# Optimization experiments

Hardware: AMD Instinct MI355X
Metric: run time of the kernel (lower is better)

The kernel has to match this reference:

```python
import jax, jax.numpy as jnp
import numpy as np

EMBED = 2048
HEADS = 16
GROUPS = 4
HEAD_DIM = EMBED // HEADS  # 128
REPEATS = HEADS // GROUPS  # 4


def setup_inputs() -> dict:
    key = jax.random.key(0)
    ks = jax.random.split(key, 9)
    s = 1.0 / np.sqrt(EMBED)
    kv_dim = GROUPS * HEAD_DIM
    return {
        "x": jax.random.normal(ks[0], (2, 2048, EMBED), dtype=jnp.float32),
        "Wq": jax.random.normal(ks[1], (EMBED, EMBED), dtype=jnp.float32) * s,
        "bq": jnp.zeros((EMBED,), dtype=jnp.float32),
        "Wk": jax.random.normal(ks[2], (EMBED, kv_dim), dtype=jnp.float32) * s,
        "bk": jnp.zeros((kv_dim,), dtype=jnp.float32),
        "Wv": jax.random.normal(ks[3], (EMBED, kv_dim), dtype=jnp.float32) * s,
        "bv": jnp.zeros((kv_dim,), dtype=jnp.float32),
        "Wo": jax.random.normal(ks[4], (EMBED, EMBED), dtype=jnp.float32) * s,
        "bo": jnp.zeros((EMBED,), dtype=jnp.float32),
    }


def reference(x, Wq, bq, Wk, bk, Wv, bv, Wo, bo):
    b, t, e = x.shape
    q = x @ Wq + bq                                   # [b,t,e]
    k = x @ Wk + bk                                   # [b,t,g*d]
    v = x @ Wv + bv
    # [b, g, r, t, d] for q; [b, g, t, d] for k,v (repeat_interleave == group-major)
    q = q.reshape(b, t, GROUPS, REPEATS, HEAD_DIM).transpose(0, 2, 3, 1, 4)
    k = k.reshape(b, t, GROUPS, HEAD_DIM).transpose(0, 2, 1, 3)
    v = v.reshape(b, t, GROUPS, HEAD_DIM).transpose(0, 2, 1, 3)
    scale = 1.0 / np.sqrt(HEAD_DIM)
    scores = jnp.einsum('bgrqd,bgkd->bgrqk', q, k) * scale
    causal = jnp.tril(jnp.ones((t, t), dtype=bool))
    scores = jnp.where(causal, scores, -jnp.inf)
    w = jax.nn.softmax(scores, axis=-1)
    out = jnp.einsum('bgrqk,bgkd->bgrqd', w, v)       # [b,g,r,t,d]
    out = out.transpose(0, 3, 1, 2, 4).reshape(b, t, e)
    return out @ Wo + bo
```

## Files before the change

kernel.cpp:

```cpp
#include <hip/hip_runtime.h>
#include <cstdint>

typedef __bf16 bf16;
typedef __attribute__((ext_vector_type(8))) __bf16 bf16x8;
typedef __attribute__((ext_vector_type(4))) __bf16 bf16x4;
typedef __attribute__((ext_vector_type(4))) float f32x4;
typedef __attribute__((ext_vector_type(4))) short short4_t;

__device__ __forceinline__ void load_lds16(const void* g, void* l) {
  __builtin_amdgcn_global_load_lds(
      (const __attribute__((address_space(1))) unsigned int*)g,
      (__attribute__((address_space(3))) unsigned int*)l, 16, 0, 0);
}

__device__ __forceinline__ float fast_exp2(float x) {
  float r;
  asm volatile("v_exp_f32 %0, %1" : "=v"(r) : "v"(x));
  return r;
}

template <bool OUT_F32>
__global__ __launch_bounds__(256) void gemm_bt(
    const bf16* __restrict__ A, const bf16* __restrict__ Bt,
    const float* __restrict__ bias, void* __restrict__ Cv,
    int M, int N, int K) {
  __shared__ __align__(16) bf16 sA[128 * 64];
  __shared__ __align__(16) bf16 sB[128 * 64];
  const int t = threadIdx.x;
  const int w = t >> 6, lane = t & 63;
  const int quad = lane >> 4, l16 = lane & 15;
  const int wm = (w >> 1) * 64, wn = (w & 1) * 64;
  const int nbx = gridDim.x;
  const int nwg = nbx * gridDim.y;
  const int orig = blockIdx.y * nbx + blockIdx.x;
  const int id = (orig & 7) * (nwg >> 3) + (orig >> 3);
  const int bm = (id / nbx) * 128, bn = (id % nbx) * 128;

  f32x4 acc[4][4] = {};
  const int srow = lane >> 3;
  const int sg = lane & 7;

  for (int kt = 0; kt < (K >> 6); ++kt) {
    const int k0 = kt << 6;
#pragma unroll
    for (int c2 = 0; c2 < 4; ++c2) {
      int c = c2 * 4 + w;
      int row = c * 8 + srow;
      int gg = sg ^ (row & 7);
      load_lds16(A + (int64_t)(bm + row) * K + k0 + gg * 8, sA + c * 512);
      load_lds16(Bt + (int64_t)(bn + row) * K + k0 + gg * 8, sB + c * 512);
    }
    asm volatile("s_waitcnt vmcnt(0)" ::: "memory");
    __syncthreads();
#pragma unroll
    for (int ks = 0; ks < 2; ++ks) {
      bf16x8 af[4], bfr[4];
#pragma unroll
      for (int i = 0; i < 4; ++i) {
        int m = wm + i * 16 + l16;
        af[i] = *(const bf16x8*)(sA + m * 64 + (((ks * 4 + quad) ^ (l16 & 7)) * 8));
        int n = wn + i * 16 + l16;
        bfr[i] = *(const bf16x8*)(sB + n * 64 + (((ks * 4 + quad) ^ (l16 & 7)) * 8));
      }
#pragma unroll
      for (int i = 0; i < 4; ++i)
#pragma unroll
        for (int j = 0; j < 4; ++j)
          acc[i][j] = __builtin_amdgcn_mfma_f32_16x16x32_bf16(af[i], bfr[j],
                                                              acc[i][j], 0, 0, 0);
    }
    __syncthreads();
  }
#pragma unroll
  for (int i = 0; i < 4; ++i) {
    int gm = bm + wm + i * 16 + quad * 4;
#pragma unroll
    for (int j = 0; j < 4; ++j) {
      int gn = bn + wn + j * 16 + l16;
      float bvv = bias ? bias[gn] : 0.0f;
#pragma unroll
      for (int r = 0; r < 4; ++r) {
        float v = acc[i][j][r] + bvv;
        if (OUT_F32)
          ((float*)Cv)[(int64_t)(gm + r) * N + gn] = v;
        else
          ((bf16*)Cv)[(int64_t)(gm + r) * N + gn] = (bf16)v;
      }
    }
  }
}

__global__ __launch_bounds__(256, 2) void attn(
    const bf16* __restrict__ QKV, const bf16* __restrict__ Vt,
    bf16* __restrict__ Out) {
  constexpr float CC = 0.08838834764831845f * 1.44269504088896f;
  __shared__ __align__(16) bf16 sK[2][64 * 128];
  __shared__ __align__(16) bf16 sV[2][128 * 64];

  const int t = threadIdx.x;
  const int w = t >> 6, lane = t & 63;
  const int quad = lane >> 4, l16 = lane & 15;
  const int h = blockIdx.y, b = blockIdx.z;
  const int p = (b == 0) ? (int)blockIdx.x : 15 - (int)blockIdx.x;
  const int g = h >> 2;
  const int wr0 = w * 16;
  const int kbase = 2048 + g * 128;
  const bf16* vtb = Vt + (int64_t)((b * 4 + g) * 128) * 2048;
  const int rk = lane >> 4, rv = lane >> 3, sgv = lane & 7;
  const int qrow0A = p * 64, qrow0B = (31 - p) * 64;
  const int niters = 32 - p;

  auto stage = [&](int n0, bf16* sKb, bf16* sVb) {
#pragma unroll
    for (int c2 = 0; c2 < 4; ++c2) {
      int c = c2 * 4 + w;
      int rowk = c * 4 + rk;
      int ggk = (l16 & 8) | ((l16 ^ rowk) & 7);
      load_lds16(QKV + (int64_t)(b * 2048 + n0 + rowk) * 3072 + kbase + ggk * 8,
                 sKb + c * 512);
      int rowv = c * 8 + rv;
      int ggv = sgv ^ (rowv & 7);
      load_lds16(vtb + (int64_t)rowv * 2048 + n0 + ggv * 8, sVb + c * 512);
    }
  };

  stage(0, sK[0], sV[0]);

  bf16x8 qreg[2][4];
#pragma unroll
  for (int u = 0; u < 2; ++u) {
    int qr = (u == 0 ? qrow0A : qrow0B);
#pragma unroll
    for (int ks = 0; ks < 4; ++ks) {
      bf16x8 v = *(const bf16x8*)(QKV +
          (int64_t)(b * 2048 + qr + wr0 + l16) * 3072 + h * 128 + ks * 32 +
          quad * 8);
#pragma unroll
      for (int e = 0; e < 8; ++e) v[e] = (bf16)((float)v[e] * CC);
      qreg[u][ks] = v;
    }
  }

  f32x4 oacc[2][8] = {};
  float mrow[2] = {-3.0e38f, -3.0e38f};
  float lrow[2] = {0.f, 0.f};

  for (int it = 0; it < niters; ++it) {
    const int cur = it & 1;
    const int n0 = it * 64;
    bf16* sKc = sK[cur];
    bf16* sVc = sV[cur];
    const bool actA = (it <= p);

    asm volatile("s_waitcnt vmcnt(0)\n\ts_barrier" ::: "memory");
    if (it + 1 < niters) stage(n0 + 64, sK[cur ^ 1], sV[cur ^ 1]);

    f32x4 sacc[2][4] = {};
    if (actA) {
#pragma unroll
      for (int ks = 0; ks < 4; ++ks) {
        bf16x8 ak[4];
#pragma unroll
        for (int mj = 0; mj < 4; ++mj) {
          int kvr = mj * 16 + l16;
          int G = ks * 4 + quad;
          int slot = (G & 8) | ((G ^ kvr) & 7);
          ak[mj] = *(const bf16x8*)(sKc + kvr * 128 + slot * 8);
        }
        __builtin_amdgcn_s_setprio(1);
#pragma unroll
        for (int mj = 0; mj < 4; ++mj) {
          sacc[0][mj] = __builtin_amdgcn_mfma_f32_16x16x32_bf16(
              ak[mj], qreg[0][ks], sacc[0][mj], 0, 0, 0);
          sacc[1][mj] = __builtin_amdgcn_mfma_f32_16x16x32_bf16(
              ak[mj], qreg[1][ks], sacc[1][mj], 0, 0, 0);
        }
        __builtin_amdgcn_s_setprio(0);
      }
    } else {
#pragma unroll
      for (int ks = 0; ks < 4; ++ks) {
        bf16x8 ak[4];
#pragma unroll
        for (int mj = 0; mj < 4; ++mj) {
          int kvr = mj * 16 + l16;
          int G = ks * 4 + quad;
          int slot = (G & 8) | ((G ^ kvr) & 7);
          ak[mj] = *(const bf16x8*)(sKc + kvr * 128 + slot * 8);
        }
        __builtin_amdgcn_s_setprio(1);
#pragma unroll
        for (int mj = 0; mj < 4; ++mj)
          sacc[1][mj] = __builtin_amdgcn_mfma_f32_16x16x32_bf16(
              ak[mj], qreg[1][ks], sacc[1][mj], 0, 0, 0);
        __builtin_amdgcn_s_setprio(0);
      }
    }

    short4_t pb[2][4];
    auto softmax_u = [&](int u, bool last, int qrow0u) {
      if (last) {
        int qg = qrow0u + wr0 + l16;
#pragma unroll
        for (int mj = 0; mj < 4; ++mj)
#pragma unroll
          for (int r = 0; r < 4; ++r) {
            int kv = n0 + mj * 16 + quad * 4 + r;
            if (kv > qg) sacc[u][mj][r] = -3.0e38f;
          }
      }
      f32x4 m01, m23;
#pragma unroll
      for (int r = 0; r < 4; ++r) {
        m01[r] = fmaxf(sacc[u][0][r], sacc[u][1][r]);
        m23[r] = fmaxf(sacc[u][2][r], sacc[u][3][r]);
      }
      float mx = fmaxf(fmaxf(fmaxf(m01[0], m01[1]), fmaxf(m01[2], m01[3])),
                       fmaxf(fmaxf(m23[0], m23[1]), fmaxf(m23[2], m23[3])));
      mx = fmaxf(mx, __shfl_xor(mx, 16));
      mx = fmaxf(mx, __shfl_xor(mx, 32));
      if (!__all(mx <= mrow[u] + 11.0f)) {
        float mnew = fmaxf(mrow[u], mx);
        float alpha = fast_exp2(mrow[u] - mnew);
        lrow[u] *= alpha;
#pragma unroll
        for (int dj = 0; dj < 8; ++dj)
#pragma unroll
          for (int r = 0; r < 4; ++r) oacc[u][dj][r] *= alpha;
        mrow[u] = mnew;
      }
      float rs = 0.f;
#pragma unroll
      for (int mj = 0; mj < 4; ++mj) {
        bf16x4 p4;
#pragma unroll
        for (int r = 0; r < 4; ++r) {
          float pv = fast_exp2(sacc[u][mj][r] - mrow[u]);
          rs += pv;
          p4[r] = (bf16)pv;
        }
        pb[u][mj] = __builtin_bit_cast(short4_t, p4);
      }
      rs += __shfl_xor(rs, 16);
      rs += __shfl_xor(rs, 32);
      lrow[u] += rs;
    };
    if (actA) softmax_u(0, it == p, qrow0A);
    softmax_u(1, it == niters - 1, qrow0B);

#pragma unroll
    for (int mj = 0; mj < 4; ++mj) {
      const int sbase = mj * 2 + (quad >> 1);
      const int soff = (quad & 1) * 4;
      short4_t av[8];
#pragma unroll
      for (int dj = 0; dj < 8; ++dj) {
        int d = dj * 16 + l16;
        av[dj] = *(const short4_t*)(sVc + d * 64 + ((sbase ^ (d & 7)) * 8) + soff);
      }
      __builtin_amdgcn_s_setprio(1);
      if (actA) {
#pragma unroll
        for (int dj = 0; dj < 8; ++dj) {
          oacc[0][dj] = __builtin_amdgcn_mfma_f32_16x16x16bf16_1k(
              av[dj], pb[0][mj], oacc[0][dj], 0, 0, 0);
          oacc[1][dj] = __builtin_amdgcn_mfma_f32_16x16x16bf16_1k(
              av[dj], pb[1][mj], oacc[1][dj], 0, 0, 0);
        }
      } else {
#pragma unroll
        for (int dj = 0; dj < 8; ++dj)
          oacc[1][dj] = __builtin_amdgcn_mfma_f32_16x16x16bf16_1k(
              av[dj], pb[1][mj], oacc[1][dj], 0, 0, 0);
      }
      __builtin_amdgcn_s_setprio(0);
    }
  }

#pragma unroll
  for (int u = 0; u < 2; ++u) {
    int qrow0u = (u == 0 ? qrow0A : qrow0B);
    float inv = 1.0f / lrow[u];
    int64_t grow = b * 2048 + qrow0u + wr0 + l16;
#pragma unroll
    for (int dj = 0; dj < 8; ++dj) {
      bf16x4 o4;
#pragma unroll
      for (int r = 0; r < 4; ++r) o4[r] = (bf16)(oacc[u][dj][r] * inv);
      *(bf16x4*)(Out + grow * 2048 + h * 128 + dj * 16 + quad * 4) = o4;
    }
  }
}

__device__ __forceinline__ void tr_tile(const float* __restrict__ W,
                                        bf16* __restrict__ Wt, int K, int N,
                                        int bx, int by, int t, float* tile) {
  int tx = t & 63, ty = t >> 6;
#pragma unroll
  for (int q2 = 0; q2 < 16; ++q2) {
    int r = ty + q2 * 4;
    tile[r * 65 + tx] = W[(int64_t)(by * 64 + r) * N + bx * 64 + tx];
  }
  __syncthreads();
#pragma unroll
  for (int q2 = 0; q2 < 16; ++q2) {
    int n = ty + q2 * 4;
    Wt[(int64_t)(bx * 64 + n) * K + by * 64 + tx] = (bf16)tile[tx * 65 + n];
  }
}

__global__ __launch_bounds__(256) void prep(
    const float* __restrict__ x, const float* __restrict__ Wq,
    const float* __restrict__ Wk, const float* __restrict__ Wv,
    const float* __restrict__ Wo, const float* __restrict__ bq,
    const float* __restrict__ bk, const float* __restrict__ bv,
    bf16* __restrict__ xb, bf16* __restrict__ wqkvT, bf16* __restrict__ woT,
    float* __restrict__ bqkv) {
  __shared__ float tile[64 * 65];
  const int bid = blockIdx.x;
  const int t = threadIdx.x;
  if (bid < 8192) {
    int idx = bid * 256 + t;
    float4 v = ((const float4*)x)[idx];
    bf16x4 o = {(bf16)v.x, (bf16)v.y, (bf16)v.z, (bf16)v.w};
    ((bf16x4*)xb)[idx] = o;
  } else if (bid < 8192 + 1024) {
    int b2 = bid - 8192;
    tr_tile(Wq, wqkvT, 2048, 2048, b2 & 31, b2 >> 5, t, tile);
  } else if (bid < 8192 + 1024 + 256) {
    int b2 = bid - (8192 + 1024);
    tr_tile(Wk, wqkvT + 2048 * 2048, 2048, 512, b2 & 7, b2 >> 3, t, tile);
  } else if (bid < 8192 + 1024 + 512) {
    int b2 = bid - (8192 + 1024 + 256);
    tr_tile(Wv, wqkvT + 2560 * 2048, 2048, 512, b2 & 7, b2 >> 3, t, tile);
  } else if (bid < 8192 + 1024 + 512 + 1024) {
    int b2 = bid - (8192 + 1024 + 512);
    tr_tile(Wo, woT, 2048, 2048, b2 & 31, b2 >> 5, t, tile);
  } else {
    int i = (bid - (8192 + 1024 + 512 + 1024)) * 256 + t;
    if (i < 3072)
      bqkv[i] = i < 2048 ? bq[i] : (i < 2560 ? bk[i - 2048] : bv[i - 2560]);
  }
}

__global__ void transpose_v(const bf16* __restrict__ QKV, bf16* __restrict__ Vt) {
  __shared__ bf16 tile[32][34];
  int dt = blockIdx.x, tt = blockIdx.y, bg = blockIdx.z;
  int b = bg >> 2, g = bg & 3;
  int tx = threadIdx.x, ty = threadIdx.y;
#pragma unroll
  for (int q2 = 0; q2 < 4; ++q2) {
    int trow = tt * 32 + ty + q2 * 8;
    tile[ty + q2 * 8][tx] =
        QKV[(int64_t)(b * 2048 + trow) * 3072 + 2560 + g * 128 + dt * 32 + tx];
  }
  __syncthreads();
#pragma unroll
  for (int q2 = 0; q2 < 4; ++q2) {
    int d = dt * 32 + ty + q2 * 8;
    Vt[(int64_t)(bg * 128 + d) * 2048 + tt * 32 + tx] = tile[tx][ty + q2 * 8];
  }
}

extern "C" void kernel_launch(void* const* d_in, const int* in_sizes, int n_in,
                              void* d_out, int out_size, void* d_ws,
                              size_t ws_size, hipStream_t stream) {
  const float* x = (const float*)d_in[0];
  const float* Wq = (const float*)d_in[1];
  const float* bq = (const float*)d_in[2];
  const float* Wk = (const float*)d_in[3];
  const float* bk = (const float*)d_in[4];
  const float* Wv = (const float*)d_in[5];
  const float* bv = (const float*)d_in[6];
  const float* Wo = (const float*)d_in[7];
  const float* bo = (const float*)d_in[8];
  float* out = (float*)d_out;

  char* ws = (char*)d_ws;
  bf16* xb = (bf16*)(ws);
  bf16* wqkvT = (bf16*)(ws + 16777216);
  bf16* woT = (bf16*)(ws + 29360128);
  float* bqkv = (float*)(ws + 37748736);
  bf16* qkv = (bf16*)(ws + 37761024);
  bf16* vt = (bf16*)(ws + 62926848);
  bf16* attnb = (bf16*)(ws + 67121152);

  prep<<<8192 + 1024 + 512 + 1024 + 12, 256, 0, stream>>>(
      x, Wq, Wk, Wv, Wo, bq, bk, bv, xb, wqkvT, woT, bqkv);

  gemm_bt<false><<<dim3(24, 32), 256, 0, stream>>>(xb, wqkvT, bqkv, qkv, 4096,
                                                   3072, 2048);
  transpose_v<<<dim3(4, 64, 8), dim3(32, 8), 0, stream>>>(qkv, vt);
  attn<<<dim3(16, 16, 2), 256, 0, stream>>>(qkv, vt, attnb);
  gemm_bt<true><<<dim3(16, 32), 256, 0, stream>>>(attnb, woT, bo, out, 4096,
                                                  2048, 2048);
}
```

Before: 308.2 us.

## Fuse V transpose into QKV GEMM epilogue and drop workgroup swizzle

The QKV projection GEMM now writes the V columns directly in transposed layout through an LDS staging tile in its epilogue, which removes the separate transpose_v kernel launch and its extra read/write of V. The LDS buffer is merged and enlarged (padded stride 136) for the staging step. The change also removes the XCD-aware workgroup remapping and uses plain blockIdx tile mapping. That could hurt L2 locality across the chiplets and offset the gain from the fusion.

```diff
diff --git a/kernel.cpp b/kernel.cpp
--- a/kernel.cpp
+++ b/kernel.cpp
@@ -19,22 +19,19 @@
   return r;
 }
 
-template <bool OUT_F32>
+template <bool OUT_F32, bool VSPLIT>
 __global__ __launch_bounds__(256) void gemm_bt(
     const bf16* __restrict__ A, const bf16* __restrict__ Bt,
     const float* __restrict__ bias, void* __restrict__ Cv,
-    int M, int N, int K) {
-  __shared__ __align__(16) bf16 sA[128 * 64];
-  __shared__ __align__(16) bf16 sB[128 * 64];
+    int M, int N, int K, bf16* __restrict__ Vt) {
+  __shared__ __align__(16) bf16 smem[VSPLIT ? 128 * 136 : 128 * 128];
+  bf16* sA = smem;
+  bf16* sB = smem + 128 * 64;
   const int t = threadIdx.x;
   const int w = t >> 6, lane = t & 63;
   const int quad = lane >> 4, l16 = lane & 15;
   const int wm = (w >> 1) * 64, wn = (w & 1) * 64;
-  const int nbx = gridDim.x;
-  const int nwg = nbx * gridDim.y;
-  const int orig = blockIdx.y * nbx + blockIdx.x;
-  const int id = (orig & 7) * (nwg >> 3) + (orig >> 3);
-  const int bm = (id / nbx) * 128, bn = (id % nbx) * 128;
+  const int bm = blockIdx.y * 128, bn = blockIdx.x * 128;
 
   f32x4 acc[4][4] = {};
   const int srow = lane >> 3;
@@ -71,6 +68,34 @@
     }
     __syncthreads();
   }
+
+  if (VSPLIT && bn >= 2560) {
+#pragma unroll
+    for (int i = 0; i < 4; ++i) {
+      int m0 = wm + i * 16 + quad * 4;
+#pragma unroll
+      for (int j = 0; j < 4; ++j) {
+        int n_l = wn + j * 16 + l16;
+        float bvv = bias ? bias[bn + n_l] : 0.0f;
+        bf16x4 o4;
+#pragma unroll
+        for (int r = 0; r < 4; ++r) o4[r] = (bf16)(acc[i][j][r] + bvv);
+        *(bf16x4*)(smem + n_l * 136 + m0) = o4;
+      }
+    }
+    __syncthreads();
+    const int n_l = t >> 1, half = t & 1;
+    const int g = (bn - 2560) >> 7;
+    const int b2 = bm >> 11;
+    const int t0 = (bm & 2047) + half * 64;
+    bf16* dst = Vt + ((int64_t)((b2 * 4 + g) * 128 + n_l)) * 2048 + t0;
+    const bf16* src = smem + n_l * 136 + half * 64;
+#pragma unroll
+    for (int c = 0; c < 8; ++c)
+      *(bf16x8*)(dst + c * 8) = *(const bf16x8*)(src + c * 8);
+    return;
+  }
+
 #pragma unroll
   for (int i = 0; i < 4; ++i) {
     int gm = bm + wm + i * 16 + quad * 4;
@@ -343,25 +368,6 @@
   }
 }
 
-__global__ void transpose_v(const bf16* __restrict__ QKV, bf16* __restrict__ Vt) {
-  __shared__ bf16 tile[32][34];
-  int dt = blockIdx.x, tt = blockIdx.y, bg = blockIdx.z;
-  int b = bg >> 2, g = bg & 3;
-  int tx = threadIdx.x, ty = threadIdx.y;
-#pragma unroll
-  for (int q2 = 0; q2 < 4; ++q2) {
-    int trow = tt * 32 + ty + q2 * 8;
-    tile[ty + q2 * 8][tx] =
-        QKV[(int64_t)(b * 2048 + trow) * 3072 + 2560 + g * 128 + dt * 32 + tx];
-  }
-  __syncthreads();
-#pragma unroll
-  for (int q2 = 0; q2 < 4; ++q2) {
-    int d = dt * 32 + ty + q2 * 8;
-    Vt[(int64_t)(bg * 128 + d) * 2048 + tt * 32 + tx] = tile[tx][ty + q2 * 8];
-  }
-}
-
 extern "C" void kernel_launch(void* const* d_in, const int* in_sizes, int n_in,
                               void* d_out, int out_size, void* d_ws,
                               size_t ws_size, hipStream_t stream) {
@@ -388,10 +394,9 @@
   prep<<<8192 + 1024 + 512 + 1024 + 12, 256, 0, stream>>>(
       x, Wq, Wk, Wv, Wo, bq, bk, bv, xb, wqkvT, woT, bqkv);
 
-  gemm_bt<false><<<dim3(24, 32), 256, 0, stream>>>(xb, wqkvT, bqkv, qkv, 4096,
-                                                   3072, 2048);
-  transpose_v<<<dim3(4, 64, 8), dim3(32, 8), 0, stream>>>(qkv, vt);
+  gemm_bt<false, true><<<dim3(24, 32), 256, 0, stream>>>(
+      xb, wqkvT, bqkv, qkv, 4096, 3072, 2048, vt);
   attn<<<dim3(16, 16, 2), 256, 0, stream>>>(qkv, vt, attnb);
-  gemm_bt<true><<<dim3(16, 32), 256, 0, stream>>>(attnb, woT, bo, out, 4096,
-                                                  2048, 2048);
-}
+  gemm_bt<true, false><<<dim3(16, 32), 256, 0, stream>>>(
+      attnb, woT, bo, out, 4096, 2048, 2048, nullptr);
+}
```

Result: faster. 297.7 us (-3.4%).
